# Kernel optimization log

Measured on AMD Instinct MI355X. Metric: run time of the kernel, lower is better.

Reference implementation:

```python
import jax, jax.numpy as jnp
import numpy as np


def setup_inputs() -> dict:
    key = jax.random.key(0)
    ks = jax.random.split(key, 7)
    b, h, w, c = 4, 64, 64, 256
    fc = 64
    s = 0.05  # small init so exp(-d^2) and softmax stay well-conditioned
    return {
        "feature_map": jax.random.normal(ks[0], (b, h, w, c), dtype=jnp.float32),
        "W_emb": jax.random.normal(ks[1], (fc, c), dtype=jnp.float32) * s,
        "b_emb": jax.random.normal(ks[2], (fc,), dtype=jnp.float32) * s,
        "W_att": jax.random.normal(ks[3], (c, c), dtype=jnp.float32) * s,
        "b_att": jax.random.normal(ks[4], (c,), dtype=jnp.float32) * s,
        "W_thr": jax.random.normal(ks[5], (1, c), dtype=jnp.float32) * s,
        "b_thr": jax.random.normal(ks[6], (1,), dtype=jnp.float32) * s,
        "layer": 0,
    }


def reference(feature_map, W_emb, b_emb, W_att, b_att, W_thr, b_thr, layer):
    # feature_map: (b, h, w, c) channels-last (torch permutes to NCHW; 1x1 convs
    # are pointwise matmuls, so we stay channels-last).
    b, h, w, c = feature_map.shape
    hw = h * w

    # embeddings_conv (1x1): (b,h,w,c) @ (c,fc) -> (b,hw,fc)
    emb = (jnp.einsum('bhwc,fc->bhwf', feature_map, W_emb) + b_emb).reshape(b, hw, -1)

    # ||ei - ej||^2 via expansion (avoids (b,hw,hw,fc) broadcast)
    sq_norm = jnp.sum(emb * emb, axis=-1)  # (b, hw)
    sq_dist = sq_norm[:, :, None] + sq_norm[:, None, :] - 2.0 * jnp.einsum('bif,bjf->bij', emb, emb)
    sq_dist = jnp.maximum(sq_dist, 0.0)
    sim = jnp.exp(-sq_dist)  # (b, hw, hw)

    # attention_conv (1x1)
    shortcut = jnp.einsum('bhwc,dc->bhwd', feature_map, W_att) + b_att  # (b,h,w,c)
    # instance_threshold_conv (1x1) on shortcut -> (b, hw)
    Tinst = (jnp.einsum('bhwc,oc->bhwo', shortcut, W_thr) + b_thr).reshape(b, hw)

    A = jnp.maximum(sim - Tinst[:, None, :], 0.0)
    A = jax.nn.softmax(A, axis=1)  # torch Softmax(dim=1) on (b, hw, hw)

    sc_flat = shortcut.reshape(b, hw, c)  # (b, hw, c)
    # torch: bmm(shortcut(b,c,hw), A^T) -> out[b,c,i] = sum_j sc[b,c,j] * A[b,i,j]
    inst = jnp.einsum('bjc,bij->bic', sc_flat, A).reshape(b, h, w, c)

    return feature_map + inst  # (b, h, w, c)
```

## Files before the change

### kernel.cpp

```cpp
#include <hip/hip_runtime.h>
#include <hip/hip_bf16.h>
#include <math.h>

typedef __attribute__((ext_vector_type(8))) short short8;
typedef __attribute__((ext_vector_type(4))) short s16x4;
typedef __attribute__((ext_vector_type(4))) float f32x4;

#define BB 4
#define HW 4096
#define CC 256
#define FC 64
#define L2E 1.4426950408889634f

#define OFF_EMB   0
#define OFF_SCT2  (2*1024*1024)
#define OFF_SQN   (OFF_SCT2 + 8*1024*1024)
#define OFF_T     (OFF_SQN + 65536)
#define OFF_D     (OFF_T   + 65536)
#define OFF_WEMB2 (OFF_D   + 65536)
#define OFF_WATT2 (OFF_WEMB2 + 32768)

static __device__ __forceinline__ short f2bf(float f) {
    __hip_bfloat16 h = __float2bfloat16(f);
    return *reinterpret_cast<short*>(&h);
}
static __device__ __forceinline__ float bf2f(short s) {
    __hip_bfloat16 h = *reinterpret_cast<__hip_bfloat16*>(&s);
    return __bfloat162float(h);
}
static __device__ __forceinline__ float fexp2(float x) {
#if __has_builtin(__builtin_amdgcn_exp2f)
    return __builtin_amdgcn_exp2f(x);
#else
    float r; asm("v_exp_f32 %0, %1" : "=v"(r) : "v"(x)); return r;
#endif
}
static __device__ __forceinline__ float frcp(float x) {
#if __has_builtin(__builtin_amdgcn_rcpf)
    return __builtin_amdgcn_rcpf(x);
#else
    return 1.0f / x;
#endif
}
static __device__ __forceinline__ short xf1(float dot, float sq, float tt,
                                            float id, float sni) {
    float x1 = fminf(fmaf(dot, 2.f*L2E, fmaf(-L2E, sq, sni)), 0.f);
    float e1 = fexp2(x1);
    float a_ = fmaxf(fmaf(e1, L2E, -L2E*tt), 0.f);
    return f2bf(fexp2(a_) * id);
}

__global__ __launch_bounds__(256) void k_prep(const float* __restrict__ Wemb,
    const float* __restrict__ Watt, short* __restrict__ Wemb2,
    short* __restrict__ Watt2, float* __restrict__ D)
{
    const int bid = blockIdx.x, t = threadIdx.x;
    if (bid < 256) {
        Watt2[(size_t)(t>>3)*2048 + bid*8 + (t&7)] = f2bf(Watt[(size_t)bid*256 + t]);
        if (bid < 64) D[bid*256 + t] = 0.f;
    } else {
        const int f = bid - 256;
        Wemb2[(size_t)(t>>3)*512 + f*8 + (t&7)] = f2bf(Wemb[(size_t)f*256 + t]);
    }
}

__global__ __launch_bounds__(256) void k_front(const float* __restrict__ fm,
    const short* __restrict__ Wemb2, const short* __restrict__ Watt2,
    const float* __restrict__ bemb, const float* __restrict__ batt,
    const float* __restrict__ wthr, const float* __restrict__ bthr,
    short* __restrict__ emb, short* __restrict__ sct2,
    float* __restrict__ sqn, float* __restrict__ T)
{
    const int blk = blockIdx.x;
    const int b = blk >> 8;
    const int r0 = (blk & 255) * 16;
    const int t = threadIdx.x;
    const int w = t >> 6, lane = t & 63, g = lane >> 4, n16 = lane & 15;
    __shared__ short fmt[16*256];
    __shared__ float tred[16][4];
    __shared__ float qred[16][4];
    #pragma unroll
    for (int v = t; v < 512; v += 256) {
        const int row = v >> 5, c32 = v & 31;
        const float4* src = (const float4*)(fm + ((size_t)b*HW + r0 + row)*CC + c32*8);
        float4 x0 = src[0], x1 = src[1];
        short8 pv;
        pv[0]=f2bf(x0.x); pv[1]=f2bf(x0.y); pv[2]=f2bf(x0.z); pv[3]=f2bf(x0.w);
        pv[4]=f2bf(x1.x); pv[5]=f2bf(x1.y); pv[6]=f2bf(x1.z); pv[7]=f2bf(x1.w);
        *(short8*)((char*)fmt + row*512 + ((c32*16) ^ ((row&7)<<4))) = pv;
    }
    __syncthreads();
    const int cb = w*64, fb = w*16;
    f32x4 acc[4], acce;
    #pragma unroll
    for (int nn = 0; nn < 4; ++nn) acc[nn] = (f32x4){0.f,0.f,0.f,0.f};
    acce = (f32x4){0.f,0.f,0.f,0.f};
    #pragma unroll
    for (int kk = 0; kk < 8; ++kk) {
        const int kc = kk*4 + g;
        short8 a = *(const short8*)((const char*)fmt + n16*512 + ((kc*16) ^ ((n16&7)<<4)));
        const short* wb = Watt2 + (size_t)kc*2048 + (cb + n16)*8;
        #pragma unroll
        for (int nn = 0; nn < 4; ++nn) {
            short8 bv = *(const short8*)(wb + nn*128);
            acc[nn] = __builtin_amdgcn_mfma_f32_16x16x32_bf16(a, bv, acc[nn], 0, 0, 0);
        }
        short8 be = *(const short8*)(Wemb2 + (size_t)kc*512 + (fb + n16)*8);
        acce = __builtin_amdgcn_mfma_f32_16x16x32_bf16(a, be, acce, 0, 0, 0);
    }
    float tp[4] = {0.f,0.f,0.f,0.f};
    const int jt_ = r0 >> 6;
    const int jc0 = (r0 & 63) >> 3;
    const size_t tilebase = ((size_t)b*64 + jt_)*8;
    #pragma unroll
    for (int nn = 0; nn < 4; ++nn) {
        const int ch = cb + nn*16 + n16;
        const float ba_ = batt[ch], wt_ = wthr[ch];
        float v[4];
        #pragma unroll
        for (int r = 0; r < 4; ++r) { v[r] = acc[nn][r] + ba_; tp[r] = fmaf(v[r], wt_, tp[r]); }
        const int jc = jc0 + (g >> 1);
        const int jw0 = (g & 1)*4;
        short* dstp = sct2 + (tilebase + jc)*2048 + (size_t)ch*8;
        unsigned u01 = (unsigned short)f2bf(v[0]) | ((unsigned)(unsigned short)f2bf(v[1]) << 16);
        unsigned u23 = (unsigned short)f2bf(v[2]) | ((unsigned)(unsigned short)f2bf(v[3]) << 16);
        *(unsigned*)(dstp + jw0)     = u01;
        *(unsigned*)(dstp + jw0 + 2) = u23;
    }
    #pragma unroll
    for (int r = 0; r < 4; ++r)
        #pragma unroll
        for (int off = 1; off <= 8; off <<= 1) tp[r] += __shfl_xor(tp[r], off);
    const int f = fb + n16;
    const float be_ = bemb[f];
    float qp[4];
    #pragma unroll
    for (int r = 0; r < 4; ++r) {
        short bv = f2bf(acce[r] + be_);
        emb[((size_t)b*HW + r0 + g*4 + r)*FC + f] = bv;
        float ef = bf2f(bv);
        qp[r] = ef*ef;
        #pragma unroll
        for (int off = 1; off <= 8; off <<= 1) qp[r] += __shfl_xor(qp[r], off);
    }
    if (n16 == 0) {
        #pragma unroll
        for (int r = 0; r < 4; ++r) { tred[g*4+r][w] = tp[r]; qred[g*4+r][w] = qp[r]; }
    }
    __syncthreads();
    if (t < 16) {
        T[(size_t)b*HW + r0 + t]   = tred[t][0]+tred[t][1]+tred[t][2]+tred[t][3] + bthr[0];
        sqn[(size_t)b*HW + r0 + t] = qred[t][0]+qred[t][1]+qred[t][2]+qred[t][3];
    }
}

__global__ __launch_bounds__(256) void k_colsum(const short* __restrict__ emb,
    const float* __restrict__ sqn, const float* __restrict__ T,
    float* __restrict__ D)
{
    const int bid = blockIdx.x;
    const int split = bid & 7, jt = (bid >> 3) & 63, b = bid >> 9;
    const int t = threadIdx.x, w = t >> 6, lane = t & 63, g = lane >> 4, n16 = lane & 15;
    const size_t jbase = (size_t)b*HW + jt*64;
    __shared__ short ej[64*64];
    __shared__ short ei[2][64*64];
    __shared__ float sqni[2][64];
    #pragma unroll
    for (int v = t; v < 512; v += 256) {
        const int row = v >> 3, c8 = v & 7;
        short8 x = *(const short8*)(emb + (jbase + row)*FC + c8*8);
        *(short8*)((char*)ej + row*128 + ((c8*16) ^ ((row&7)<<4))) = x;
    }
    const int jl = w*16 + n16;
    const float sqjL = -L2E * sqn[jbase + jl];
    const float tjL  = -L2E * T[jbase + jl];
    const int srow0 = t >> 3, srow1 = (t >> 3) + 32, sc8 = t & 7;
    const int sb0 = srow0*128 + ((sc8*16) ^ ((srow0&7)<<4));
    const int sb1 = srow1*128 + ((sc8*16) ^ ((srow1&7)<<4));
    const size_t base0 = (size_t)b*HW + (size_t)split*512;
    short8 stg0 = *(const short8*)(emb + (base0 + srow0)*FC + sc8*8);
    short8 stg1 = *(const short8*)(emb + (base0 + srow1)*FC + sc8*8);
    float stgq = (t < 64) ? sqn[base0 + t] : 0.f;
    *(short8*)((char*)ei[0] + sb0) = stg0;
    *(short8*)((char*)ei[0] + sb1) = stg1;
    if (t < 64) sqni[0][t] = stgq;
    stg0 = *(const short8*)(emb + (base0 + 64 + srow0)*FC + sc8*8);
    stg1 = *(const short8*)(emb + (base0 + 64 + srow1)*FC + sc8*8);
    stgq = (t < 64) ? sqn[base0 + 64 + t] : 0.f;
    __syncthreads();
    const short8 bf0 = *(const short8*)((const char*)ej + jl*128 + ((g*16)     ^ ((jl&7)<<4)));
    const short8 bf1 = *(const short8*)((const char*)ej + jl*128 + (((g+4)*16) ^ ((jl&7)<<4)));
    float csum = 0.f;
    for (int it = 0; it < 8; ++it) {
        if (it < 7) {
            char* eib = (char*)ei[(it+1)&1];
            *(short8*)(eib + sb0) = stg0;
            *(short8*)(eib + sb1) = stg1;
            if (t < 64) sqni[(it+1)&1][t] = stgq;
            if (it < 6) {
                const size_t nb = base0 + (size_t)(it+2)*64;
                stg0 = *(const short8*)(emb + (nb + srow0)*FC + sc8*8);
                stg1 = *(const short8*)(emb + (nb + srow1)*FC + sc8*8);
                stgq = (t < 64) ? sqn[nb + t] : 0.f;
            }
        }
        const char* eib = (const char*)ei[it&1];
        const float* sqc = sqni[it&1];
        #pragma unroll
        for (int m = 0; m < 4; ++m) {
            const int arow = m*16 + n16;
            short8 a0 = *(const short8*)(eib + arow*128 + ((g*16)     ^ ((arow&7)<<4)));
            short8 a1 = *(const short8*)(eib + arow*128 + (((g+4)*16) ^ ((arow&7)<<4)));
            f32x4 dot = {0.f,0.f,0.f,0.f};
            dot = __builtin_amdgcn_mfma_f32_16x16x32_bf16(a0, bf0, dot, 0, 0, 0);
            dot = __builtin_amdgcn_mfma_f32_16x16x32_bf16(a1, bf1, dot, 0, 0, 0);
            #pragma unroll
            for (int r = 0; r < 4; ++r) {
                float x1 = fminf(fmaf(dot[r], 2.f*L2E, fmaf(-L2E, sqc[m*16 + g*4 + r], sqjL)), 0.f);
                float e1 = fexp2(x1);
                float a_ = fmaxf(fmaf(e1, L2E, tjL), 0.f);
                csum += fexp2(a_);
            }
        }
        __syncthreads();
    }
    csum += __shfl_xor(csum, 16);
    csum += __shfl_xor(csum, 32);
    if (lane < 16) atomicAdd(&D[jbase + jl], csum);
}

#define ATTN_ITER(K, bfC, sqC, tC, dC, bfN, sqN, tN, dN)                         \
  {                                                                              \
    const int kn = (K) < 63 ? (K) + 1 : 63;                                      \
    const size_t jbn = bbase + (size_t)kn * 64;                                  \
    sqN = sqn[jbn + jl]; tN = T[jbn + jl]; dN = D[jbn + jl];                     \
    {                                                                            \
      const short* sbn = sct2 + ((size_t)(b*64 + kn)*8)*2048 + (size_t)(w*64 + n16)*8; \
      _Pragma("unroll")                                                          \
      for (int nn = 0; nn < 4; ++nn) {                                           \
        _Pragma("unroll")                                                        \
        for (int kc = 0; kc < 2; ++kc)                                           \
          bfN[nn*2+kc] = *(const short8*)(sbn + (size_t)(kc*4+g)*2048 + nn*128); \
      }                                                                          \
    }                                                                            \
    {                                                                            \
      const float iD   = frcp(dC);                                               \
      const float sqjL = -L2E * sqC;                                             \
      const float tjL  = -L2E * tC;                                              \
      const char* ejb = (const char*)ejlds[(K)&1];                               \
      char* Pb = (char*)Plds[(K)&1];                                             \
      short8 b0 = *(const short8*)(ejb + jl*128 + ((g*16)     ^ ((jl&7)<<4)));   \
      short8 b1 = *(const short8*)(ejb + jl*128 + (((g+4)*16) ^ ((jl&7)<<4)));   \
      _Pragma("unroll")                                                          \
      for (int t2 = 0; t2 < 2; ++t2) {                                           \
        f32x4 dot = {0.f,0.f,0.f,0.f};                                           \
        dot = __builtin_amdgcn_mfma_f32_16x16x32_bf16(aQ0[t2], b0, dot, 0,0,0);  \
        dot = __builtin_amdgcn_mfma_f32_16x16x32_bf16(aQ1[t2], b1, dot, 0,0,0);  \
        _Pragma("unroll")                                                        \
        for (int r = 0; r < 4; ++r) {                                            \
          float x1 = fminf(fmaf(dot[r], 2.f*L2E, snL[t2][r] + sqjL), 0.f);       \
          float e1 = fexp2(x1);                                                  \
          float a_ = fmaxf(fmaf(e1, L2E, tjL), 0.f);                             \
          float p  = fexp2(a_) * iD;                                             \
          const int prow = t2*16 + g*4 + r;                                      \
          *(short*)(Pb + prow*128 + (((jl>>3) ^ (prow&7))<<4) + (jl&7)*2) = f2bf(p); \
        }                                                                        \
      }                                                                          \
    }                                                                            \
    if ((K) < 63) {                                                              \
      *(short8*)((char*)ejlds[((K)+1)&1] + sbyte0) = stg0;                       \
      *(short8*)((char*)ejlds[((K)+1)&1] + sbyte1) = stg1;                       \
      const int k2n = (K) < 62 ? (K) + 2 : 63;                                   \
      stg0 = *(const short8*)(emb + (bbase + (size_t)k2n*64 + srow0)*FC + sc8*8); \
      stg1 = *(const short8*)(emb + (bbase + (size_t)k2n*64 + srow1)*FC + sc8*8); \
    }                                                                            \
    __syncthreads();                                                             \
    {                                                                            \
      const char* Pb = (const char*)Plds[(K)&1];                                 \
      _Pragma("unroll")                                                          \
      for (int m = 0; m < 2; ++m) {                                              \
        const int prow = m*16 + n16;                                             \
        short8 pa0 = *(const short8*)(Pb + prow*128 + (((0*4+g)<<4) ^ ((prow&7)<<4))); \
        short8 pa1 = *(const short8*)(Pb + prow*128 + (((1*4+g)<<4) ^ ((prow&7)<<4))); \
        _Pragma("unroll")                                                        \
        for (int nn = 0; nn < 4; ++nn) {                                         \
          acc[m][nn] = __builtin_amdgcn_mfma_f32_16x16x32_bf16(pa0, bfC[nn*2+0], acc[m][nn], 0,0,0); \
          acc[m][nn] = __builtin_amdgcn_mfma_f32_16x16x32_bf16(pa1, bfC[nn*2+1], acc[m][nn], 0,0,0); \
        }                                                                        \
      }                                                                          \
    }                                                                            \
  }

__global__ __launch_bounds__(256, 2) void k_attn(const float* __restrict__ fm,
    const short* __restrict__ emb, const float* __restrict__ sqn,
    const float* __restrict__ T, const float* __restrict__ D,
    const short* __restrict__ sct2, float* __restrict__ out)
{
    const int bid = ((blockIdx.x & 7) << 6) | (blockIdx.x >> 3);
    const int b = bid >> 7;
    const int i0 = (bid & 127) * 32;
    const int t = threadIdx.x, w = t >> 6, lane = t & 63, g = lane >> 4, n16 = lane & 15;
    const size_t bbase = (size_t)b * HW;
    const size_t ibase = bbase + i0;
    __shared__ short ejlds[2][64*64];
    __shared__ short Plds[2][32*64];

    const int jl = w*16 + n16;

    short8 aQ0[2], aQ1[2];
    float snL[2][4];
    #pragma unroll
    for (int t2 = 0; t2 < 2; ++t2) {
        const size_t qr = ibase + t2*16 + n16;
        aQ0[t2] = *(const short8*)(emb + qr*FC + g*8);
        aQ1[t2] = *(const short8*)(emb + qr*FC + 32 + g*8);
        #pragma unroll
        for (int r = 0; r < 4; ++r)
            snL[t2][r] = -L2E * sqn[ibase + t2*16 + g*4 + r];
    }
    const int srow0 = t >> 3, srow1 = (t >> 3) + 32, sc8 = t & 7;
    const int sbyte0 = srow0*128 + ((sc8*16) ^ ((srow0&7)<<4));
    const int sbyte1 = srow1*128 + ((sc8*16) ^ ((srow1&7)<<4));
    short8 stg0 = *(const short8*)(emb + (bbase + srow0)*FC + sc8*8);
    short8 stg1 = *(const short8*)(emb + (bbase + srow1)*FC + sc8*8);
    *(short8*)((char*)ejlds[0] + sbyte0) = stg0;
    *(short8*)((char*)ejlds[0] + sbyte1) = stg1;
    stg0 = *(const short8*)(emb + (bbase + 64 + srow0)*FC + sc8*8);
    stg1 = *(const short8*)(emb + (bbase + 64 + srow1)*FC + sc8*8);

    const float sq0 = sqn[bbase + jl], t0q = T[bbase + jl], d0q = D[bbase + jl];
    float sqA, tA, dA, sqB, tB, dB;
    sqA = sqn[bbase + 64 + jl]; tA = T[bbase + 64 + jl]; dA = D[bbase + 64 + jl];
    short8 bfA[8], bfB[8];
    {
        const short* sb0 = sct2 + ((size_t)(b*64)*8)*2048 + (size_t)(w*64 + n16)*8;
        #pragma unroll
        for (int nn = 0; nn < 4; ++nn)
            #pragma unroll
            for (int kc = 0; kc < 2; ++kc)
                bfA[nn*2+kc] = *(const short8*)(sb0 + (size_t)(kc*4+g)*2048 + nn*128);
    }
    f32x4 acc[2][4];
    #pragma unroll
    for (int m = 0; m < 2; ++m)
        #pragma unroll
        for (int nn = 0; nn < 4; ++nn) acc[m][nn] = (f32x4){0.f,0.f,0.f,0.f};
    __syncthreads();

    {
        const char* ejb = (const char*)ejlds[0];
        char* Pb = (char*)Plds[0];
        const float iD = frcp(d0q);
        const float sqjL = -L2E * sq0;
        const float tjL  = -L2E * t0q;
        short8 b0 = *(const short8*)(ejb + jl*128 + ((g*16)     ^ ((jl&7)<<4)));
        short8 b1 = *(const short8*)(ejb + jl*128 + (((g+4)*16) ^ ((jl&7)<<4)));
        #pragma unroll
        for (int t2 = 0; t2 < 2; ++t2) {
            f32x4 dot = {0.f,0.f,0.f,0.f};
            dot = __builtin_amdgcn_mfma_f32_16x16x32_bf16(aQ0[t2], b0, dot, 0,0,0);
            dot = __builtin_amdgcn_mfma_f32_16x16x32_bf16(aQ1[t2], b1, dot, 0,0,0);
            #pragma unroll
            for (int r = 0; r < 4; ++r) {
                float x1 = fminf(fmaf(dot[r], 2.f*L2E, snL[t2][r] + sqjL), 0.f);
                float e1 = fexp2(x1);
                float a_ = fmaxf(fmaf(e1, L2E, tjL), 0.f);
                float p  = fexp2(a_) * iD;
                const int prow = t2*16 + g*4 + r;
                *(short*)(Pb + prow*128 + (((jl>>3) ^ (prow&7))<<4) + (jl&7)*2) = f2bf(p);
            }
        }
        *(short8*)((char*)ejlds[1] + sbyte0) = stg0;
        *(short8*)((char*)ejlds[1] + sbyte1) = stg1;
        stg0 = *(const short8*)(emb + (bbase + 128 + srow0)*FC + sc8*8);
        stg1 = *(const short8*)(emb + (bbase + 128 + srow1)*FC + sc8*8);
        __syncthreads();
    }

    for (int k2 = 0; k2 < 62; k2 += 2) {
        ATTN_ITER(k2,   bfA, sqA, tA, dA, bfB, sqB, tB, dB);
        ATTN_ITER(k2+1, bfB, sqB, tB, dB, bfA, sqA, tA, dA);
    }
    ATTN_ITER(62, bfA, sqA, tA, dA, bfB, sqB, tB, dB);

    {
        const char* Pb = (const char*)Plds[1];
        #pragma unroll
        for (int m = 0; m < 2; ++m) {
            const int prow = m*16 + n16;
            short8 pa0 = *(const short8*)(Pb + prow*128 + (((0*4+g)<<4) ^ ((prow&7)<<4)));
            short8 pa1 = *(const short8*)(Pb + prow*128 + (((1*4+g)<<4) ^ ((prow&7)<<4)));
            #pragma unroll
            for (int nn = 0; nn < 4; ++nn) {
                acc[m][nn] = __builtin_amdgcn_mfma_f32_16x16x32_bf16(pa0, bfB[nn*2+0], acc[m][nn], 0,0,0);
                acc[m][nn] = __builtin_amdgcn_mfma_f32_16x16x32_bf16(pa1, bfB[nn*2+1], acc[m][nn], 0,0,0);
            }
        }
    }

    #pragma unroll
    for (int m = 0; m < 2; ++m)
        #pragma unroll
        for (int r = 0; r < 4; ++r) {
            const size_t row = ibase + m*16 + g*4 + r;
            #pragma unroll
            for (int nn = 0; nn < 4; ++nn) {
                const size_t idx = row*CC + w*64 + nn*16 + n16;
                out[idx] = fm[idx] + acc[m][nn][r];
            }
        }
}

extern "C" void kernel_launch(void* const* d_in, const int* in_sizes, int n_in,
                              void* d_out, int out_size, void* d_ws, size_t ws_size,
                              hipStream_t stream)
{
    const float* fm   = (const float*)d_in[0];
    const float* Wemb = (const float*)d_in[1];
    const float* bemb = (const float*)d_in[2];
    const float* Watt = (const float*)d_in[3];
    const float* batt = (const float*)d_in[4];
    const float* Wthr = (const float*)d_in[5];
    const float* bthr = (const float*)d_in[6];
    char* ws = (char*)d_ws;
    short* emb   = (short*)(ws + OFF_EMB);
    short* sct2  = (short*)(ws + OFF_SCT2);
    float* sqn   = (float*)(ws + OFF_SQN);
    float* T     = (float*)(ws + OFF_T);
    float* D     = (float*)(ws + OFF_D);
    short* Wemb2 = (short*)(ws + OFF_WEMB2);
    short* Watt2 = (short*)(ws + OFF_WATT2);
    float* out = (float*)d_out;

    k_prep  <<<320,  256, 0, stream>>>(Wemb, Watt, Wemb2, Watt2, D);
    k_front <<<1024, 256, 0, stream>>>(fm, Wemb2, Watt2, bemb, batt, Wthr, bthr,
                                       emb, sct2, sqn, T);
    k_colsum<<<2048, 256, 0, stream>>>(emb, sqn, T, D);
    k_attn  <<<512,  256, 0, stream>>>(fm, emb, sqn, T, D, sct2, out);
}
```

Before: 111.2 us.

## Software-pipeline attention loop so PV of previous tile overlaps current exp

Restructures the attention main loop so that each window computes the QK dot products for tile K, then runs the P·V MFMAs for tile K-1 from the other P buffer, and only then does the exp/softmax math and writes P for tile K. This needs one barrier per window instead of a mid-iteration barrier between the P write and the PV read. The intent is to overlap the matrix-core PV work with the transcendental VALU work and to drop a sync per tile. In exchange it keeps more live registers (two dot accumulators plus both B-fragment sets) and changes the prologue and epilogue indexing, which raises the risk of register spills or off-by-one errors.

Result: no change. 110.2 us (-0.9%).

```diff
diff --git a/kernel.cpp b/kernel.cpp
--- a/kernel.cpp
+++ b/kernel.cpp
@@ -3,7 +3,6 @@
 #include <math.h>
 
 typedef __attribute__((ext_vector_type(8))) short short8;
-typedef __attribute__((ext_vector_type(4))) short s16x4;
 typedef __attribute__((ext_vector_type(4))) float f32x4;
 
 #define BB 4
@@ -42,13 +41,7 @@
     return 1.0f / x;
 #endif
 }
-static __device__ __forceinline__ short xf1(float dot, float sq, float tt,
-                                            float id, float sni) {
-    float x1 = fminf(fmaf(dot, 2.f*L2E, fmaf(-L2E, sq, sni)), 0.f);
-    float e1 = fexp2(x1);
-    float a_ = fmaxf(fmaf(e1, L2E, -L2E*tt), 0.f);
-    return f2bf(fexp2(a_) * id);
-}
+#define MFMA32(a, b, c) __builtin_amdgcn_mfma_f32_16x16x32_bf16(a, b, c, 0, 0, 0)
 
 __global__ __launch_bounds__(256) void k_prep(const float* __restrict__ Wemb,
     const float* __restrict__ Watt, short* __restrict__ Wemb2,
@@ -103,10 +96,10 @@
         #pragma unroll
         for (int nn = 0; nn < 4; ++nn) {
             short8 bv = *(const short8*)(wb + nn*128);
-            acc[nn] = __builtin_amdgcn_mfma_f32_16x16x32_bf16(a, bv, acc[nn], 0, 0, 0);
+            acc[nn] = MFMA32(a, bv, acc[nn]);
         }
         short8 be = *(const short8*)(Wemb2 + (size_t)kc*512 + (fb + n16)*8);
-        acce = __builtin_amdgcn_mfma_f32_16x16x32_bf16(a, be, acce, 0, 0, 0);
+        acce = MFMA32(a, be, acce);
     }
     float tp[4] = {0.f,0.f,0.f,0.f};
     const int jt_ = r0 >> 6;
@@ -212,8 +205,8 @@
             short8 a0 = *(const short8*)(eib + arow*128 + ((g*16)     ^ ((arow&7)<<4)));
             short8 a1 = *(const short8*)(eib + arow*128 + (((g+4)*16) ^ ((arow&7)<<4)));
             f32x4 dot = {0.f,0.f,0.f,0.f};
-            dot = __builtin_amdgcn_mfma_f32_16x16x32_bf16(a0, bf0, dot, 0, 0, 0);
-            dot = __builtin_amdgcn_mfma_f32_16x16x32_bf16(a1, bf1, dot, 0, 0, 0);
+            dot = MFMA32(a0, bf0, dot);
+            dot = MFMA32(a1, bf1, dot);
             #pragma unroll
             for (int r = 0; r < 4; ++r) {
                 float x1 = fminf(fmaf(dot[r], 2.f*L2E, fmaf(-L2E, sqc[m*16 + g*4 + r], sqjL)), 0.f);
@@ -229,66 +222,75 @@
     if (lane < 16) atomicAdd(&D[jbase + jl], csum);
 }
 
-#define ATTN_ITER(K, bfC, sqC, tC, dC, bfN, sqN, tN, dN)                         \
-  {                                                                              \
-    const int kn = (K) < 63 ? (K) + 1 : 63;                                      \
-    const size_t jbn = bbase + (size_t)kn * 64;                                  \
-    sqN = sqn[jbn + jl]; tN = T[jbn + jl]; dN = D[jbn + jl];                     \
-    {                                                                            \
-      const short* sbn = sct2 + ((size_t)(b*64 + kn)*8)*2048 + (size_t)(w*64 + n16)*8; \
-      _Pragma("unroll")                                                          \
-      for (int nn = 0; nn < 4; ++nn) {                                           \
-        _Pragma("unroll")                                                        \
-        for (int kc = 0; kc < 2; ++kc)                                           \
-          bfN[nn*2+kc] = *(const short8*)(sbn + (size_t)(kc*4+g)*2048 + nn*128); \
-      }                                                                          \
-    }                                                                            \
-    {                                                                            \
-      const float iD   = frcp(dC);                                               \
-      const float sqjL = -L2E * sqC;                                             \
-      const float tjL  = -L2E * tC;                                              \
-      const char* ejb = (const char*)ejlds[(K)&1];                               \
-      char* Pb = (char*)Plds[(K)&1];                                             \
-      short8 b0 = *(const short8*)(ejb + jl*128 + ((g*16)     ^ ((jl&7)<<4)));   \
-      short8 b1 = *(const short8*)(ejb + jl*128 + (((g+4)*16) ^ ((jl&7)<<4)));   \
-      _Pragma("unroll")                                                          \
-      for (int t2 = 0; t2 < 2; ++t2) {                                           \
-        f32x4 dot = {0.f,0.f,0.f,0.f};                                           \
-        dot = __builtin_amdgcn_mfma_f32_16x16x32_bf16(aQ0[t2], b0, dot, 0,0,0);  \
-        dot = __builtin_amdgcn_mfma_f32_16x16x32_bf16(aQ1[t2], b1, dot, 0,0,0);  \
-        _Pragma("unroll")                                                        \
-        for (int r = 0; r < 4; ++r) {                                            \
-          float x1 = fminf(fmaf(dot[r], 2.f*L2E, snL[t2][r] + sqjL), 0.f);       \
-          float e1 = fexp2(x1);                                                  \
-          float a_ = fmaxf(fmaf(e1, L2E, tjL), 0.f);                             \
-          float p  = fexp2(a_) * iD;                                             \
-          const int prow = t2*16 + g*4 + r;                                      \
-          *(short*)(Pb + prow*128 + (((jl>>3) ^ (prow&7))<<4) + (jl&7)*2) = f2bf(p); \
-        }                                                                        \
-      }                                                                          \
-    }                                                                            \
-    if ((K) < 63) {                                                              \
-      *(short8*)((char*)ejlds[((K)+1)&1] + sbyte0) = stg0;                       \
-      *(short8*)((char*)ejlds[((K)+1)&1] + sbyte1) = stg1;                       \
-      const int k2n = (K) < 62 ? (K) + 2 : 63;                                   \
-      stg0 = *(const short8*)(emb + (bbase + (size_t)k2n*64 + srow0)*FC + sc8*8); \
-      stg1 = *(const short8*)(emb + (bbase + (size_t)k2n*64 + srow1)*FC + sc8*8); \
-    }                                                                            \
-    __syncthreads();                                                             \
-    {                                                                            \
-      const char* Pb = (const char*)Plds[(K)&1];                                 \
-      _Pragma("unroll")                                                          \
-      for (int m = 0; m < 2; ++m) {                                              \
-        const int prow = m*16 + n16;                                             \
-        short8 pa0 = *(const short8*)(Pb + prow*128 + (((0*4+g)<<4) ^ ((prow&7)<<4))); \
-        short8 pa1 = *(const short8*)(Pb + prow*128 + (((1*4+g)<<4) ^ ((prow&7)<<4))); \
-        _Pragma("unroll")                                                        \
-        for (int nn = 0; nn < 4; ++nn) {                                         \
-          acc[m][nn] = __builtin_amdgcn_mfma_f32_16x16x32_bf16(pa0, bfC[nn*2+0], acc[m][nn], 0,0,0); \
-          acc[m][nn] = __builtin_amdgcn_mfma_f32_16x16x32_bf16(pa1, bfC[nn*2+1], acc[m][nn], 0,0,0); \
-        }                                                                        \
-      }                                                                          \
-    }                                                                            \
+#define WIN(K, bfC, bfN, sqC, tC, dC, sqN, tN, dN, DO_PV, DO_STG)              \
+  {                                                                            \
+                          \
+    const int kn = (K) + 1 < 64 ? (K) + 1 : 63;                                \
+    sqN = sqn[bbase + (size_t)kn*64 + jl];                                     \
+    tN  = T  [bbase + (size_t)kn*64 + jl];                                     \
+    dN  = D  [bbase + (size_t)kn*64 + jl];                                     \
+    { const short* sb_ = sct2 + ((size_t)(b*64 + (K))*8)*2048                  \
+                              + (size_t)(w*64 + n16)*8;                        \
+      _Pragma("unroll")                                                        \
+      for (int nn = 0; nn < 4; ++nn)                                           \
+        _Pragma("unroll")                                                      \
+        for (int kc = 0; kc < 2; ++kc)                                         \
+          bfN[nn*2+kc] = *(const short8*)(sb_ + (size_t)(kc*4+g)*2048 + nn*128); } \
+                                                          \
+    const char* ejb = (const char*)ejlds[(K)&1];                               \
+    short8 b0 = *(const short8*)(ejb + jl*128 + ((g*16)     ^ ((jl&7)<<4)));   \
+    short8 b1 = *(const short8*)(ejb + jl*128 + (((g+4)*16) ^ ((jl&7)<<4)));   \
+    f32x4 dot0 = {0.f,0.f,0.f,0.f}, dot1 = {0.f,0.f,0.f,0.f};                  \
+    dot0 = MFMA32(aQ0[0], b0, dot0); dot0 = MFMA32(aQ1[0], b1, dot0);          \
+    dot1 = MFMA32(aQ0[1], b0, dot1); dot1 = MFMA32(aQ1[1], b1, dot1);          \
+                            \
+    if (DO_PV) {                                                               \
+      const char* Pb = (const char*)Plds[((K)+1)&1];                           \
+      _Pragma("unroll")                                                        \
+      for (int m = 0; m < 2; ++m) {                                            \
+        const int prow = m*16 + n16;                                           \
+        short8 pa0 = *(const short8*)(Pb + prow*128 + (((0*4+g) ^ (prow&7))<<4)); \
+        short8 pa1 = *(const short8*)(Pb + prow*128 + (((1*4+g) ^ (prow&7))<<4)); \
+        _Pragma("unroll")                                                      \
+        for (int nn = 0; nn < 4; ++nn) {                                       \
+          acc[m][nn] = MFMA32(pa0, bfC[nn*2+0], acc[m][nn]);                   \
+          acc[m][nn] = MFMA32(pa1, bfC[nn*2+1], acc[m][nn]);                   \
+        }                                                                      \
+      }                                                                        \
+    }                                                                          \
+              \
+    if (DO_STG) {                                                              \
+      *(short8*)((char*)ejlds[((K)+1)&1] + sbyte0) = stg0;                     \
+      *(short8*)((char*)ejlds[((K)+1)&1] + sbyte1) = stg1;                     \
+      if ((K) + 2 < 64) {                                                      \
+        stg0 = *(const short8*)(emb + (bbase + (size_t)((K)+2)*64 + srow0)*FC + sc8*8); \
+        stg1 = *(const short8*)(emb + (bbase + (size_t)((K)+2)*64 + srow1)*FC + sc8*8); \
+      }                                                                        \
+    }                                                                          \
+                                            \
+    {                                                                          \
+      const float iD   = frcp(dC);                                             \
+      const float sqjL = -L2E * sqC;                                           \
+      const float tjL  = -L2E * tC;                                            \
+      char* Pw = (char*)Plds[(K)&1];                                           \
+      _Pragma("unroll")                                                        \
+      for (int r = 0; r < 4; ++r) {                                            \
+        float x1 = fminf(fmaf(dot0[r], 2.f*L2E, snL[0][r] + sqjL), 0.f);       \
+        float a_ = fmaxf(fmaf(fexp2(x1), L2E, tjL), 0.f);                      \
+        const int prow = g*4 + r;                                              \
+        *(short*)(Pw + prow*128 + (((jl>>3) ^ (prow&7))<<4) + (jl&7)*2)        \
+            = f2bf(fexp2(a_) * iD);                                            \
+      }                                                                        \
+      _Pragma("unroll")                                                        \
+      for (int r = 0; r < 4; ++r) {                                            \
+        float x1 = fminf(fmaf(dot1[r], 2.f*L2E, snL[1][r] + sqjL), 0.f);       \
+        float a_ = fmaxf(fmaf(fexp2(x1), L2E, tjL), 0.f);                      \
+        const int prow = 16 + g*4 + r;                                         \
+        *(short*)(Pw + prow*128 + (((jl>>3) ^ (prow&7))<<4) + (jl&7)*2)        \
+            = f2bf(fexp2(a_) * iD);                                            \
+      }                                                                        \
+    }                                                                          \
+    __syncthreads();                                                           \
   }
 
 __global__ __launch_bounds__(256, 2) void k_attn(const float* __restrict__ fm,
@@ -321,25 +323,16 @@
     const int srow0 = t >> 3, srow1 = (t >> 3) + 32, sc8 = t & 7;
     const int sbyte0 = srow0*128 + ((sc8*16) ^ ((srow0&7)<<4));
     const int sbyte1 = srow1*128 + ((sc8*16) ^ ((srow1&7)<<4));
+
     short8 stg0 = *(const short8*)(emb + (bbase + srow0)*FC + sc8*8);
     short8 stg1 = *(const short8*)(emb + (bbase + srow1)*FC + sc8*8);
     *(short8*)((char*)ejlds[0] + sbyte0) = stg0;
     *(short8*)((char*)ejlds[0] + sbyte1) = stg1;
     stg0 = *(const short8*)(emb + (bbase + 64 + srow0)*FC + sc8*8);
     stg1 = *(const short8*)(emb + (bbase + 64 + srow1)*FC + sc8*8);
-
-    const float sq0 = sqn[bbase + jl], t0q = T[bbase + jl], d0q = D[bbase + jl];
-    float sqA, tA, dA, sqB, tB, dB;
-    sqA = sqn[bbase + 64 + jl]; tA = T[bbase + 64 + jl]; dA = D[bbase + 64 + jl];
+    float sqA = sqn[bbase + jl], tA = T[bbase + jl], dA = D[bbase + jl];
+    float sqB, tB, dB;
     short8 bfA[8], bfB[8];
-    {
-        const short* sb0 = sct2 + ((size_t)(b*64)*8)*2048 + (size_t)(w*64 + n16)*8;
-        #pragma unroll
-        for (int nn = 0; nn < 4; ++nn)
-            #pragma unroll
-            for (int kc = 0; kc < 2; ++kc)
-                bfA[nn*2+kc] = *(const short8*)(sb0 + (size_t)(kc*4+g)*2048 + nn*128);
-    }
     f32x4 acc[2][4];
     #pragma unroll
     for (int m = 0; m < 2; ++m)
@@ -347,53 +340,24 @@
         for (int nn = 0; nn < 4; ++nn) acc[m][nn] = (f32x4){0.f,0.f,0.f,0.f};
     __syncthreads();
 
-    {
-        const char* ejb = (const char*)ejlds[0];
-        char* Pb = (char*)Plds[0];
-        const float iD = frcp(d0q);
-        const float sqjL = -L2E * sq0;
-        const float tjL  = -L2E * t0q;
-        short8 b0 = *(const short8*)(ejb + jl*128 + ((g*16)     ^ ((jl&7)<<4)));
-        short8 b1 = *(const short8*)(ejb + jl*128 + (((g+4)*16) ^ ((jl&7)<<4)));
-        #pragma unroll
-        for (int t2 = 0; t2 < 2; ++t2) {
-            f32x4 dot = {0.f,0.f,0.f,0.f};
-            dot = __builtin_amdgcn_mfma_f32_16x16x32_bf16(aQ0[t2], b0, dot, 0,0,0);
-            dot = __builtin_amdgcn_mfma_f32_16x16x32_bf16(aQ1[t2], b1, dot, 0,0,0);
-            #pragma unroll
-            for (int r = 0; r < 4; ++r) {
-                float x1 = fminf(fmaf(dot[r], 2.f*L2E, snL[t2][r] + sqjL), 0.f);
-                float e1 = fexp2(x1);
-                float a_ = fmaxf(fmaf(e1, L2E, tjL), 0.f);
-                float p  = fexp2(a_) * iD;
-                const int prow = t2*16 + g*4 + r;
-                *(short*)(Pb + prow*128 + (((jl>>3) ^ (prow&7))<<4) + (jl&7)*2) = f2bf(p);
-            }
-        }
-        *(short8*)((char*)ejlds[1] + sbyte0) = stg0;
-        *(short8*)((char*)ejlds[1] + sbyte1) = stg1;
-        stg0 = *(const short8*)(emb + (bbase + 128 + srow0)*FC + sc8*8);
-        stg1 = *(const short8*)(emb + (bbase + 128 + srow1)*FC + sc8*8);
-        __syncthreads();
-    }
-
-    for (int k2 = 0; k2 < 62; k2 += 2) {
-        ATTN_ITER(k2,   bfA, sqA, tA, dA, bfB, sqB, tB, dB);
-        ATTN_ITER(k2+1, bfB, sqB, tB, dB, bfA, sqA, tA, dA);
-    }
-    ATTN_ITER(62, bfA, sqA, tA, dA, bfB, sqB, tB, dB);
+    WIN(0, bfB, bfA, sqA, tA, dA, sqB, tB, dB, 0, 1)
+    for (int k = 1; k < 62; k += 2) {
+        WIN(k,   bfA, bfB, sqB, tB, dB, sqA, tA, dA, 1, 1)
+        WIN(k+1, bfB, bfA, sqA, tA, dA, sqB, tB, dB, 1, 1)
+    }
+    WIN(63, bfA, bfB, sqB, tB, dB, sqA, tA, dA, 1, 0)
 
     {
         const char* Pb = (const char*)Plds[1];
         #pragma unroll
         for (int m = 0; m < 2; ++m) {
             const int prow = m*16 + n16;
-            short8 pa0 = *(const short8*)(Pb + prow*128 + (((0*4+g)<<4) ^ ((prow&7)<<4)));
-            short8 pa1 = *(const short8*)(Pb + prow*128 + (((1*4+g)<<4) ^ ((prow&7)<<4)));
+            short8 pa0 = *(const short8*)(Pb + prow*128 + (((0*4+g) ^ (prow&7))<<4));
+            short8 pa1 = *(const short8*)(Pb + prow*128 + (((1*4+g) ^ (prow&7))<<4));
             #pragma unroll
             for (int nn = 0; nn < 4; ++nn) {
-                acc[m][nn] = __builtin_amdgcn_mfma_f32_16x16x32_bf16(pa0, bfB[nn*2+0], acc[m][nn], 0,0,0);
-                acc[m][nn] = __builtin_amdgcn_mfma_f32_16x16x32_bf16(pa1, bfB[nn*2+1], acc[m][nn], 0,0,0);
+                acc[m][nn] = MFMA32(pa0, bfB[nn*2+0], acc[m][nn]);
+                acc[m][nn] = MFMA32(pa1, bfB[nn*2+1], acc[m][nn]);
             }
         }
     }
```
